# Optimization experiments

Measured on AMD Instinct MI355X. Metric: run time of the kernel, lower is better.

## Reference

```python
import jax, jax.numpy as jnp
import numpy as np

N_X, N_UNITS, N_Y, N_U = 64, 256, 32, 64
BATCH = 32768


def setup_inputs() -> dict:
    key = jax.random.key(0)
    ks = jax.random.split(key, 10)
    nz = 2 * N_X + N_UNITS
    return {
        "u": jax.random.normal(ks[0], (BATCH, N_U, 1), dtype=jnp.float32),
        "x0": jax.random.normal(ks[1], (BATCH, N_X, 1), dtype=jnp.float32),
        # learned parameters (scaled down so H stays well-conditioned and tanh unsaturated)
        "B_2": 0.1 * jax.random.normal(ks[2], (N_X, N_U), dtype=jnp.float32),
        "C_2": 0.1 * jax.random.normal(ks[3], (N_Y, N_X), dtype=jnp.float32),
        "D_12": 0.1 * jax.random.normal(ks[4], (N_UNITS, N_U), dtype=jnp.float32),
        "D_21": 0.1 * jax.random.normal(ks[5], (N_Y, N_UNITS), dtype=jnp.float32),
        "b": 0.1 * jax.random.normal(ks[6], (N_X + N_UNITS + N_Y, 1), dtype=jnp.float32),
        "X": (1.0 / np.sqrt(nz)) * jax.random.normal(ks[7], (nz, nz), dtype=jnp.float32),
        "Y1": 0.1 * jax.random.normal(ks[8], (N_X, N_X), dtype=jnp.float32),
        # fixed IQC multipliers (train_qsr=False): Q nsd, R=I so Rinv=I; S stored transposed
        "S_t": 0.1 * jax.random.normal(ks[9], (N_U, N_Y), dtype=jnp.float32),
        "Q": -jnp.eye(N_Y, dtype=jnp.float32),
        "Rinv": jnp.eye(N_U, dtype=jnp.float32),
    }


def _constrained_weights(B_2, C_2, D_12, D_21, X, S_t, Q, Rinv):
    """Port of REN.updateConstrainedWeights (train_qsr=False). Returns C_1, D_11, lam."""
    n_x, n_units = B_2.shape[0], D_12.shape[0]
    n_y = C_2.shape[0]
    nz = 2 * n_x + n_units
    C2_ = S_t @ C_2                       # [n_u, n_x]
    D21_ = S_t @ D_21 - D_12.T            # [n_u, n_units]
    H = X.T @ X + 1e-3 * jnp.eye(nz, dtype=X.dtype)
    lT1 = jnp.concatenate([C2_.T, D21_.T, B_2], axis=0)          # [nz, n_u]
    H = H + lT1 @ Rinv @ lT1.T
    lT2 = jnp.concatenate([C_2.T, D_21.T, jnp.zeros((n_x, n_y), dtype=X.dtype)], axis=0)
    H = H - lT2 @ Q @ lT2.T
    H_21 = H[n_x:n_x + n_units, :n_x]
    H_22 = H[n_x:n_x + n_units, n_x:n_x + n_units]
    C_1 = -H_21                           # [n_units, n_x]
    lam = 0.5 * jnp.diag(H_22)            # Lambda diagonal, > 0 since H is PD
    # L = tril(-(H_22 - diag(H_22))) == -strictly_lower(H_22)
    D_11 = -jnp.tril(H_22, k=-1)          # strictly lower triangular [n_units, n_units]
    return C_1, D_11, lam


def _forward(u, x0, B_2, C_2, D_12, D_21, b, X, Y1, S_t, Q, Rinv):
    n_x, n_units = B_2.shape[0], D_12.shape[0]
    C_1, D_11, lam = _constrained_weights(B_2, C_2, D_12, D_21, X, S_t, Q, Rinv)
    u2 = u[:, :, 0]                       # [B, n_u]
    x2 = x0[:, :, 0]                      # [B, n_x]
    b_w = b[n_x:n_x + n_units, 0]         # [n_units]
    b_y = b[n_x + n_units:, 0]            # [n_y]
    # precompute the non-recurrent part of the pre-activation for all units
    v = x2 @ C_1.T + u2 @ D_12.T + b_w    # [B, n_units]
    # NOTE: the source uses D_11 row (i_unit - 1), not i_unit (faithful to original code).
    # For i=0 the source uses term2 = 0; D_11 is strictly lower so the full-row dot
    # against the partially-filled w (zeros beyond index i) matches D_11[i-1, :i] @ w[:i].
    Drows = jnp.concatenate([jnp.zeros((1, n_units), dtype=D_11.dtype), D_11[:-1]], axis=0)
    batch = u2.shape[0]

    def step(w, i):
        wi = jnp.tanh((v[:, i] + w @ Drows[i]) / lam[i])   # [B]
        w = w.at[:, i].set(wi)
        return w, None

    w0 = jnp.zeros((batch, n_units), dtype=v.dtype)
    w, _ = jax.lax.scan(step, w0, jnp.arange(n_units))
    y = x2 @ C_2.T + w @ D_21.T + b_y     # [B, n_y]
    return y[:, :, None]                  # [B, n_y, 1]


def reference(u, x0, B_2, C_2, D_12, D_21, b, X, Y1, S_t, Q, Rinv):
    return _forward(u, x0, B_2, C_2, D_12, D_21, b, X, Y1, S_t, Q, Rinv)
```

## Files before the change

kernel.cpp:

```cpp
#include <hip/hip_runtime.h>
#include <hip/hip_bf16.h>

typedef __attribute__((ext_vector_type(8))) short short8;
typedef __attribute__((ext_vector_type(4))) float floatx4;
typedef __attribute__((ext_vector_type(2))) float floatx2;

#define MFMA16 __builtin_amdgcn_mfma_f32_16x16x32_bf16

__device__ inline unsigned short bf16_rn(float f) {
    return (unsigned short)((__float_as_uint(f) + 0x8000u) >> 16);
}
__device__ inline short8 pack8(const float* v) {
    union { short8 s; unsigned int u[4]; } r;
#pragma unroll
    for (int j = 0; j < 4; j++) {
        union { __hip_bfloat162 h; unsigned int u; } c;
        c.h = __float22bfloat162_rn(make_float2(v[2 * j], v[2 * j + 1]));
        r.u[j] = c.u;
    }
    return r.s;
}

__global__ __launch_bounds__(64) void ren_prep13(
    const float* __restrict__ B2, const float* __restrict__ C2,
    const float* __restrict__ D12, const float* __restrict__ D21,
    const float* __restrict__ St, const float* __restrict__ Q,
    const float* __restrict__ Rinv,
    float* __restrict__ lT1, float* __restrict__ t1,
    float* __restrict__ lT2, float* __restrict__ t2,
    unsigned short* __restrict__ Wvb, unsigned short* __restrict__ C2b,
    unsigned short* __restrict__ D21b)
{
    const int t = threadIdx.x;
    const int blk = blockIdx.x;
    if (blk >= 384) {
        const int id = (blk - 384) * 64 + t;
        if (id < 16384) {
            Wvb[(id >> 6) * 128 + 64 + (id & 63)] = bf16_rn(D12[id]);
        } else if (id < 16384 + 2048) {
            C2b[id - 16384] = bf16_rn(C2[id - 16384]);
        } else if (id < 16384 + 2048 + 8192) {
            D21b[id - 18432] = bf16_rn(D21[id - 18432]);
        }
        return;
    }

    __shared__ float stl[64 * 33];
    __shared__ float colbuf[32];
    __shared__ float s1[64];

    const int r = blk;
    const int c = t;
#pragma unroll
    for (int j = 0; j < 32; j++) {
        const int id = j * 64 + t;
        stl[(id >> 5) * 33 + (id & 31)] = St[id];
    }
    if (t < 32)
        colbuf[t] = (r < 64) ? C2[t * 64 + r]
                  : (r < 320 ? D21[t * 256 + (r - 64)] : 0.f);
    __syncthreads();

    float v1;
    if (r < 64) {
        float s = 0.f;
#pragma unroll
        for (int p = 0; p < 32; p++) s += stl[c * 33 + p] * colbuf[p];
        v1 = s;
    } else if (r < 320) {
        float s = 0.f;
#pragma unroll
        for (int p = 0; p < 32; p++) s += stl[c * 33 + p] * colbuf[p];
        v1 = s - D12[(r - 64) * 64 + c];
    } else {
        v1 = B2[(r - 320) * 64 + c];
    }
    s1[c] = v1;
    lT1[r * 64 + c] = v1;
    if (c < 32) {
        const float v2 = (r < 320) ? colbuf[c] : 0.f;
        lT2[r * 32 + c] = v2;
    }
    __syncthreads();

    float a = 0.f;
#pragma unroll
    for (int k = 0; k < 64; k++) a += s1[k] * Rinv[k * 64 + c];
    t1[r * 64 + c] = a;

    if (c < 32) {
        float bq = 0.f;
#pragma unroll
        for (int k = 0; k < 32; k++) bq += colbuf[k] * Q[k * 32 + c];
        t2[r * 32 + c] = bq;
    }
}

__global__ __launch_bounds__(320) void ren_prep2(
    const float* __restrict__ X,
    const float* __restrict__ lT1, const float* __restrict__ t1,
    const float* __restrict__ lT2, const float* __restrict__ t2,
    unsigned short* __restrict__ Wvb, unsigned short* __restrict__ Drowsb,
    float* __restrict__ Dpair, float* __restrict__ lamg)
{
    __shared__ float xcol[384];
    const int c = threadIdx.x;
    const int i = blockIdx.x;
    for (int t = c; t < 384; t += 320) xcol[t] = X[t * 384 + 64 + i];
    __syncthreads();

    float f0 = 0.f, f1 = 0.f, f2 = 0.f, f3 = 0.f;
    float ac[8], au[8], bc8[8], bu[8];
#pragma unroll
    for (int kk = 0; kk < 8; kk++) { ac[kk] = X[kk * 384 + c]; au[kk] = xcol[kk]; }
    for (int k0 = 0; k0 < 384; k0 += 16) {
#pragma unroll
        for (int kk = 0; kk < 8; kk++) {
            bc8[kk] = X[(k0 + 8 + kk) * 384 + c]; bu[kk] = xcol[k0 + 8 + kk];
        }
        f0 += au[0] * ac[0]; f1 += au[1] * ac[1];
        f2 += au[2] * ac[2]; f3 += au[3] * ac[3];
        f0 += au[4] * ac[4]; f1 += au[5] * ac[5];
        f2 += au[6] * ac[6]; f3 += au[7] * ac[7];
        if (k0 + 16 < 384) {
#pragma unroll
            for (int kk = 0; kk < 8; kk++) {
                ac[kk] = X[(k0 + 16 + kk) * 384 + c]; au[kk] = xcol[k0 + 16 + kk];
            }
        }
        f0 += bu[0] * bc8[0]; f1 += bu[1] * bc8[1];
        f2 += bu[2] * bc8[2]; f3 += bu[3] * bc8[3];
        f0 += bu[4] * bc8[4]; f1 += bu[5] * bc8[5];
        f2 += bu[6] * bc8[6]; f3 += bu[7] * bc8[7];
    }

    const float* __restrict__ t1r = t1 + (64 + i) * 64;
    const float* __restrict__ l1r = lT1 + c * 64;
#pragma unroll
    for (int m4 = 0; m4 < 16; m4++) {
        const float4 lv = *(const float4*)(l1r + m4 * 4);
        f0 += t1r[m4 * 4 + 0] * lv.x; f1 += t1r[m4 * 4 + 1] * lv.y;
        f2 += t1r[m4 * 4 + 2] * lv.z; f3 += t1r[m4 * 4 + 3] * lv.w;
    }
    const float* __restrict__ t2r = t2 + (64 + i) * 32;
    const float* __restrict__ l2r = lT2 + c * 32;
#pragma unroll
    for (int m4 = 0; m4 < 8; m4++) {
        const float4 lv = *(const float4*)(l2r + m4 * 4);
        f0 -= t2r[m4 * 4 + 0] * lv.x; f1 -= t2r[m4 * 4 + 1] * lv.y;
        f2 -= t2r[m4 * 4 + 2] * lv.z; f3 -= t2r[m4 * 4 + 3] * lv.w;
    }
    float acc = (f0 + f1) + (f2 + f3) + (((64 + i) == c) ? 0.001f : 0.f);

    if (c < 64) {
        Wvb[i * 128 + c] = bf16_rn(-acc);
    } else {
        const int cb = c - 64;
        if (cb == i) lamg[i] = 5.7707801635558536f / acc;
        if (i < 255) {
            const float dv = (cb <= i - 1) ? -acc : 0.f;
            Drowsb[(i + 1) * 256 + cb] = bf16_rn(dv);
            const int row = i + 1;
            if ((row >> 4) == (cb >> 4)) {
                const int q = row & 15, p = cb & 15;
                Dpair[(row >> 4) * 256 + (q >> 1) * 32 + p * 2 + (q & 1)] = dv;
            }
        } else {
            Drowsb[cb] = 0;
        }
    }
}

__global__ __launch_bounds__(64) void ren_main(
    const float* __restrict__ u, const float* __restrict__ x0,
    const float* __restrict__ b,
    const unsigned short* __restrict__ Wvb,
    const unsigned short* __restrict__ Drowsb,
    const float* __restrict__ Dpair,
    const float* __restrict__ lamg,
    const unsigned short* __restrict__ C2b,
    const unsigned short* __restrict__ D21b,
    float* __restrict__ out)
{
    __shared__ float buf[2][16][20];
    __shared__ float dblk[2][256];
    __shared__ float lamsh[256];
    __shared__ float bsh[256];

    const int L = threadIdx.x;
    const int col = L & 15;
    const int quad = L >> 4;
    const int row0 = blockIdx.x * 16;

#pragma unroll
    for (int j = 0; j < 4; j++) {
        lamsh[j * 64 + L] = lamg[j * 64 + L];
        bsh[j * 64 + L]   = b[64 + j * 64 + L];
    }

    short8 zf[4];
#pragma unroll
    for (int c = 0; c < 4; c++) {
        const float* p = (c < 2 ? x0 : u) + (long)(row0 + col) * 64 + (c & 1) * 32 + quad * 8;
        float t[8];
        *(float4*)&t[0] = *(const float4*)p;
        *(float4*)&t[4] = *(const float4*)(p + 4);
        zf[c] = pack8(t);
    }

    const short8 zero8 = {0, 0, 0, 0, 0, 0, 0, 0};
    short8 wf[8];
#pragma unroll
    for (int c = 0; c < 8; c++) wf[c] = zero8;

    float4 dcur = *(const float4*)(Dpair + 4 * L);
    floatx4 acc0 = {0.f, 0.f, 0.f, 0.f}, acc1 = {0.f, 0.f, 0.f, 0.f};
    {
        short8 v0 = *(const short8*)(Wvb + col * 128 + quad * 8);
        short8 v1 = *(const short8*)(Wvb + col * 128 + 32 + quad * 8);
        short8 v2 = *(const short8*)(Wvb + col * 128 + 64 + quad * 8);
        short8 v3 = *(const short8*)(Wvb + col * 128 + 96 + quad * 8);
        acc0 = MFMA16(zf[0], v0, acc0, 0, 0, 0);
        acc1 = MFMA16(zf[1], v1, acc1, 0, 0, 0);
        acc0 = MFMA16(zf[2], v2, acc0, 0, 0, 0);
        acc1 = MFMA16(zf[3], v3, acc1, 0, 0, 0);
    }

    short8 yc[4];

#pragma unroll
    for (int n = 0; n < 16; n++) {
        const int pp = n & 1;

        short8 vfN[4], hfN[8];
        float4 dnxt;
        if (n < 15) {
            dnxt = *(const float4*)(Dpair + (n + 1) * 256 + 4 * L);
#pragma unroll
            for (int c = 0; c < 4; c++)
                vfN[c] = *(const short8*)(Wvb + (16 * (n + 1) + col) * 128 + c * 32 + quad * 8);
#pragma unroll
            for (int c = 0; c < 8; c++)
                if (c < ((n + 2) >> 1))
                    hfN[c] = *(const short8*)(Drowsb + (16 * (n + 1) + col) * 256 + c * 32 + quad * 8);
        } else {
            yc[0] = *(const short8*)(C2b + col * 64 + quad * 8);
            yc[1] = *(const short8*)(C2b + col * 64 + 32 + quad * 8);
            yc[2] = *(const short8*)(C2b + (16 + col) * 64 + quad * 8);
            yc[3] = *(const short8*)(C2b + (16 + col) * 64 + 32 + quad * 8);
        }

        *(float4*)&dblk[pp][4 * L] = dcur;
        const float bwv = bsh[16 * n + col];
#pragma unroll
        for (int r = 0; r < 4; r++)
            buf[pp][quad * 4 + r][col] = acc0[r] + acc1[r] + bwv;

        float vl[16];
#pragma unroll
        for (int p4 = 0; p4 < 4; p4++)
            *(float4*)&vl[p4 * 4] = *(const float4*)&buf[pp][col][p4 * 4];

        float wl[16];
#pragma unroll
        for (int tq = 0; tq < 8; tq++) {
            floatx2 a2;
            a2[0] = vl[2 * tq]; a2[1] = vl[2 * tq + 1];
#pragma unroll
            for (int p4 = 0; p4 < tq; p4++) {
                const float4 d4 = *(const float4*)&dblk[pp][tq * 32 + p4 * 4];
                floatx2 de; de[0] = d4.x; de[1] = d4.y;
                floatx2 dz; dz[0] = d4.z; dz[1] = d4.w;
                a2 += de * wl[2 * p4];
                a2 += dz * wl[2 * p4 + 1];
            }
            const float2 lmp = *(const float2*)&lamsh[16 * n + 2 * tq];
            floatx2 lm2; lm2[0] = lmp.x; lm2[1] = lmp.y;
            a2 *= lm2;
            const float e0 = __builtin_amdgcn_exp2f(a2[0]);
            const float e1 = __builtin_amdgcn_exp2f(a2[1]);
            wl[2 * tq]     = 1.f - 2.f * __builtin_amdgcn_rcpf(e0 + 1.f);
            wl[2 * tq + 1] = 1.f - 2.f * __builtin_amdgcn_rcpf(e1 + 1.f);
        }

        {
            const short8 nf = pack8(&wl[(quad & 1) * 8]);
            const int cc = n >> 1;
            if ((n & 1) == 0) wf[cc] = (quad < 2) ? nf : zero8;
            else if (quad >= 2) wf[cc] = nf;
        }

        if (n < 15) {
            floatx4 a0 = {0.f, 0.f, 0.f, 0.f}, a1 = {0.f, 0.f, 0.f, 0.f};
            a0 = MFMA16(zf[0], vfN[0], a0, 0, 0, 0);
            a1 = MFMA16(zf[1], vfN[1], a1, 0, 0, 0);
            a0 = MFMA16(zf[2], vfN[2], a0, 0, 0, 0);
            a1 = MFMA16(zf[3], vfN[3], a1, 0, 0, 0);
#pragma unroll
            for (int c = 0; c < 8; c++)
                if (c < ((n + 2) >> 1)) {
                    if (c & 1) a1 = MFMA16(wf[c], hfN[c], a1, 0, 0, 0);
                    else       a0 = MFMA16(wf[c], hfN[c], a0, 0, 0, 0);
                }
            acc0 = a0; acc1 = a1;
            dcur = dnxt;
        }
    }

    floatx4 y0 = {0.f, 0.f, 0.f, 0.f}, y1 = {0.f, 0.f, 0.f, 0.f};
    y0 = MFMA16(zf[0], yc[0], y0, 0, 0, 0);
    y1 = MFMA16(zf[0], yc[2], y1, 0, 0, 0);
    y0 = MFMA16(zf[1], yc[1], y0, 0, 0, 0);
    y1 = MFMA16(zf[1], yc[3], y1, 0, 0, 0);
#pragma unroll
    for (int c = 0; c < 8; c++) {
        const short8 b0 = *(const short8*)(D21b + col * 256 + c * 32 + quad * 8);
        const short8 b1 = *(const short8*)(D21b + (16 + col) * 256 + c * 32 + quad * 8);
        y0 = MFMA16(wf[c], b0, y0, 0, 0, 0);
        y1 = MFMA16(wf[c], b1, y1, 0, 0, 0);
    }
    const float by0 = b[320 + col];
    const float by1 = b[336 + col];
#pragma unroll
    for (int r = 0; r < 4; r++) {
        out[(long)(row0 + quad * 4 + r) * 32 + col]      = y0[r] + by0;
        out[(long)(row0 + quad * 4 + r) * 32 + 16 + col] = y1[r] + by1;
    }
}

extern "C" void kernel_launch(void* const* d_in, const int* in_sizes, int n_in,
                              void* d_out, int out_size, void* d_ws, size_t ws_size,
                              hipStream_t stream)
{
    const float* u    = (const float*)d_in[0];
    const float* x0   = (const float*)d_in[1];
    const float* B2   = (const float*)d_in[2];
    const float* C2   = (const float*)d_in[3];
    const float* D12  = (const float*)d_in[4];
    const float* D21  = (const float*)d_in[5];
    const float* b    = (const float*)d_in[6];
    const float* X    = (const float*)d_in[7];
    const float* St   = (const float*)d_in[9];
    const float* Q    = (const float*)d_in[10];
    const float* Rinv = (const float*)d_in[11];
    float* out = (float*)d_out;

    float* ws     = (float*)d_ws;
    float* lT1    = ws;
    float* t1     = lT1 + 384 * 64;
    float* lT2    = t1 + 384 * 64;
    float* t2     = lT2 + 384 * 32;
    float* lamg   = t2 + 384 * 32;
    float* Dpair  = lamg + 256;
    unsigned short* Drowsb = (unsigned short*)(Dpair + 16 * 256);
    unsigned short* Wvb    = Drowsb + 256 * 256;
    unsigned short* C2b    = Wvb + 256 * 128;
    unsigned short* D21b   = C2b + 32 * 64;

    ren_prep13<<<dim3(800), dim3(64), 0, stream>>>(B2, C2, D12, D21, St, Q, Rinv,
                                                   lT1, t1, lT2, t2, Wvb, C2b, D21b);
    ren_prep2<<<dim3(256), dim3(320), 0, stream>>>(X, lT1, t1, lT2, t2,
                                                   Wvb, Drowsb, Dpair, lamg);

    const int batch = in_sizes[0] / 64;
    ren_main<<<dim3(batch / 16), dim3(64), 0, stream>>>(u, x0, b, Wvb, Drowsb,
                                                        Dpair, lamg, C2b, D21b, out);
}
```

Baseline: 141.3 us.

## Share staged weight blocks across four waves via LDS double buffering

The main kernel grows from one wave per block to four waves (256 threads). The per-step weight fragments (Wv, Drows band, Dpair) are repacked in the prep kernels into one contiguous pre-swizzled staging layout. Each block cooperatively loads the next step's slab into a double-buffered shared-memory array, and every wave reads its MFMA operands from LDS. This cuts redundant global and L2 weight traffic per batch row, at the cost of a block-wide barrier every step and more LDS per block, which may limit occupancy.

```diff
diff --git a/kernel.cpp b/kernel.cpp
--- a/kernel.cpp
+++ b/kernel.cpp
@@ -6,6 +6,8 @@
 typedef __attribute__((ext_vector_type(2))) float floatx2;
 
 #define MFMA16 __builtin_amdgcn_mfma_f32_16x16x32_bf16
+
+#define BASEF4(n) (320 * (n) + 64 * ((((n) * (n))) >> 2))
 
 __device__ inline unsigned short bf16_rn(float f) {
     return (unsigned short)((__float_as_uint(f) + 0x8000u) >> 16);
@@ -28,7 +30,7 @@
     const float* __restrict__ Rinv,
     float* __restrict__ lT1, float* __restrict__ t1,
     float* __restrict__ lT2, float* __restrict__ t2,
-    unsigned short* __restrict__ Wvb, unsigned short* __restrict__ C2b,
+    unsigned short* __restrict__ stgS, unsigned short* __restrict__ C2b,
     unsigned short* __restrict__ D21b)
 {
     const int t = threadIdx.x;
@@ -36,7 +38,11 @@
     if (blk >= 384) {
         const int id = (blk - 384) * 64 + t;
         if (id < 16384) {
-            Wvb[(id >> 6) * 128 + 64 + (id & 63)] = bf16_rn(D12[id]);
+            const int i = id >> 6, k = id & 63;
+            const int n = i >> 4, r = i & 15;
+            const int cc = 2 + (k >> 5), kk = k & 31;
+            stgS[(BASEF4(n) + cc * 64 + (kk >> 3) * 16 + r) * 8 + (kk & 7)] =
+                bf16_rn(D12[id]);
         } else if (id < 16384 + 2048) {
             C2b[id - 16384] = bf16_rn(C2[id - 16384]);
         } else if (id < 16384 + 2048 + 8192) {
@@ -100,8 +106,7 @@
     const float* __restrict__ X,
     const float* __restrict__ lT1, const float* __restrict__ t1,
     const float* __restrict__ lT2, const float* __restrict__ t2,
-    unsigned short* __restrict__ Wvb, unsigned short* __restrict__ Drowsb,
-    float* __restrict__ Dpair, float* __restrict__ lamg)
+    float* __restrict__ stgF, float* __restrict__ lamg)
 {
     __shared__ float xcol[384];
     const int c = threadIdx.x;
@@ -152,97 +157,88 @@
     }
     float acc = (f0 + f1) + (f2 + f3) + (((64 + i) == c) ? 0.001f : 0.f);
 
+    unsigned short* stgS = (unsigned short*)stgF;
     if (c < 64) {
-        Wvb[i * 128 + c] = bf16_rn(-acc);
+        const int n = i >> 4, r = i & 15;
+        const int cc = c >> 5, kk = c & 31;
+        stgS[(BASEF4(n) + cc * 64 + (kk >> 3) * 16 + r) * 8 + (kk & 7)] =
+            bf16_rn(-acc);
     } else {
         const int cb = c - 64;
         if (cb == i) lamg[i] = 5.7707801635558536f / acc;
         if (i < 255) {
+            const int row = i + 1, n = row >> 4, r = row & 15;
+            const int cN = (n + 1) >> 1;
             const float dv = (cb <= i - 1) ? -acc : 0.f;
-            Drowsb[(i + 1) * 256 + cb] = bf16_rn(dv);
-            const int row = i + 1;
-            if ((row >> 4) == (cb >> 4)) {
-                const int q = row & 15, p = cb & 15;
-                Dpair[(row >> 4) * 256 + (q >> 1) * 32 + p * 2 + (q & 1)] = dv;
-            }
-        } else {
-            Drowsb[cb] = 0;
-        }
-    }
-}
-
-__global__ __launch_bounds__(64) void ren_main(
+            if (cb < cN * 32) {
+                const int cc = cb >> 5, kk = cb & 31;
+                stgS[(BASEF4(n) + 256 + cc * 64 + (kk >> 3) * 16 + r) * 8 + (kk & 7)] =
+                    bf16_rn(dv);
+            }
+            if ((cb >> 4) == (row >> 4)) {
+                stgF[(BASEF4(n) + 256 + cN * 64) * 4 +
+                     (r >> 1) * 32 + (cb & 15) * 2 + (r & 1)] = dv;
+            }
+        }
+    }
+}
+
+__global__ __launch_bounds__(256, 2) void ren_main(
     const float* __restrict__ u, const float* __restrict__ x0,
     const float* __restrict__ b,
-    const unsigned short* __restrict__ Wvb,
-    const unsigned short* __restrict__ Drowsb,
-    const float* __restrict__ Dpair,
+    const float4* __restrict__ stg,
     const float* __restrict__ lamg,
     const unsigned short* __restrict__ C2b,
     const unsigned short* __restrict__ D21b,
     float* __restrict__ out)
 {
-    __shared__ float buf[2][16][20];
-    __shared__ float dblk[2][256];
+    __shared__ float4 sbuf[2][832];
+    __shared__ float tbuf[4][16][20];
     __shared__ float lamsh[256];
     __shared__ float bsh[256];
 
-    const int L = threadIdx.x;
-    const int col = L & 15;
-    const int quad = L >> 4;
-    const int row0 = blockIdx.x * 16;
-
-#pragma unroll
-    for (int j = 0; j < 4; j++) {
-        lamsh[j * 64 + L] = lamg[j * 64 + L];
-        bsh[j * 64 + L]   = b[64 + j * 64 + L];
-    }
+    const int tid = threadIdx.x;
+    const int L = tid & 63, wid = tid >> 6;
+    const int col = L & 15, quad = L >> 4;
+    const long row0 = (long)blockIdx.x * 64 + wid * 16;
+
+    lamsh[tid] = lamg[tid];
+    bsh[tid]   = b[64 + tid];
 
     short8 zf[4];
 #pragma unroll
     for (int c = 0; c < 4; c++) {
-        const float* p = (c < 2 ? x0 : u) + (long)(row0 + col) * 64 + (c & 1) * 32 + quad * 8;
+        const float* p = (c < 2 ? x0 : u) + (row0 + col) * 64 + (c & 1) * 32 + quad * 8;
         float t[8];
         *(float4*)&t[0] = *(const float4*)p;
         *(float4*)&t[4] = *(const float4*)(p + 4);
         zf[c] = pack8(t);
     }
 
+    sbuf[0][tid] = stg[tid];
+    if (tid < 64) sbuf[0][256 + tid] = stg[256 + tid];
+    __syncthreads();
+
     const short8 zero8 = {0, 0, 0, 0, 0, 0, 0, 0};
     short8 wf[8];
 #pragma unroll
     for (int c = 0; c < 8; c++) wf[c] = zero8;
 
-    float4 dcur = *(const float4*)(Dpair + 4 * L);
-    floatx4 acc0 = {0.f, 0.f, 0.f, 0.f}, acc1 = {0.f, 0.f, 0.f, 0.f};
-    {
-        short8 v0 = *(const short8*)(Wvb + col * 128 + quad * 8);
-        short8 v1 = *(const short8*)(Wvb + col * 128 + 32 + quad * 8);
-        short8 v2 = *(const short8*)(Wvb + col * 128 + 64 + quad * 8);
-        short8 v3 = *(const short8*)(Wvb + col * 128 + 96 + quad * 8);
-        acc0 = MFMA16(zf[0], v0, acc0, 0, 0, 0);
-        acc1 = MFMA16(zf[1], v1, acc1, 0, 0, 0);
-        acc0 = MFMA16(zf[2], v2, acc0, 0, 0, 0);
-        acc1 = MFMA16(zf[3], v3, acc1, 0, 0, 0);
-    }
-
     short8 yc[4];
 
 #pragma unroll
     for (int n = 0; n < 16; n++) {
-        const int pp = n & 1;
-
-        short8 vfN[4], hfN[8];
-        float4 dnxt;
+        const int cur = n & 1, nxt = cur ^ 1;
+        const int cN = (n + 1) >> 1;
+        if (n > 0) __syncthreads();
+
+        float4 st[4];
+        const int totN = 320 + ((n + 2) >> 1) * 64;
         if (n < 15) {
-            dnxt = *(const float4*)(Dpair + (n + 1) * 256 + 4 * L);
-#pragma unroll
-            for (int c = 0; c < 4; c++)
-                vfN[c] = *(const short8*)(Wvb + (16 * (n + 1) + col) * 128 + c * 32 + quad * 8);
-#pragma unroll
-            for (int c = 0; c < 8; c++)
-                if (c < ((n + 2) >> 1))
-                    hfN[c] = *(const short8*)(Drowsb + (16 * (n + 1) + col) * 256 + c * 32 + quad * 8);
+#pragma unroll
+            for (int r = 0; r < 4; r++)
+                if (r * 256 + tid < totN)
+                    st[r] = stg[BASEF4(n + 1) + r * 256 + tid];
         } else {
             yc[0] = *(const short8*)(C2b + col * 64 + quad * 8);
             yc[1] = *(const short8*)(C2b + col * 64 + 32 + quad * 8);
@@ -250,17 +246,37 @@
             yc[3] = *(const short8*)(C2b + (16 + col) * 64 + 32 + quad * 8);
         }
 
-        *(float4*)&dblk[pp][4 * L] = dcur;
+        const float4* sb = sbuf[cur];
+        floatx4 acc0 = {0.f, 0.f, 0.f, 0.f}, acc1 = {0.f, 0.f, 0.f, 0.f};
+        {
+            const short8 v0 = *(const short8*)&sb[0 * 64 + L];
+            const short8 v1 = *(const short8*)&sb[1 * 64 + L];
+            const short8 v2 = *(const short8*)&sb[2 * 64 + L];
+            const short8 v3 = *(const short8*)&sb[3 * 64 + L];
+            acc0 = MFMA16(zf[0], v0, acc0, 0, 0, 0);
+            acc1 = MFMA16(zf[1], v1, acc1, 0, 0, 0);
+            acc0 = MFMA16(zf[2], v2, acc0, 0, 0, 0);
+            acc1 = MFMA16(zf[3], v3, acc1, 0, 0, 0);
+        }
+#pragma unroll
+        for (int c = 0; c < 8; c++)
+            if (c < cN) {
+                const short8 hb = *(const short8*)&sb[256 + c * 64 + L];
+                if (c & 1) acc1 = MFMA16(wf[c], hb, acc1, 0, 0, 0);
+                else       acc0 = MFMA16(wf[c], hb, acc0, 0, 0, 0);
+            }
+
         const float bwv = bsh[16 * n + col];
 #pragma unroll
         for (int r = 0; r < 4; r++)
-            buf[pp][quad * 4 + r][col] = acc0[r] + acc1[r] + bwv;
+            tbuf[wid][quad * 4 + r][col] = acc0[r] + acc1[r] + bwv;
 
         float vl[16];
 #pragma unroll
         for (int p4 = 0; p4 < 4; p4++)
-            *(float4*)&vl[p4 * 4] = *(const float4*)&buf[pp][col][p4 * 4];
-
+            *(float4*)&vl[p4 * 4] = *(const float4*)&tbuf[wid][col][p4 * 4];
+
+        const float* dpr = (const float*)(sb + 256 + cN * 64);
         float wl[16];
 #pragma unroll
         for (int tq = 0; tq < 8; tq++) {
@@ -268,7 +284,7 @@
             a2[0] = vl[2 * tq]; a2[1] = vl[2 * tq + 1];
 #pragma unroll
             for (int p4 = 0; p4 < tq; p4++) {
-                const float4 d4 = *(const float4*)&dblk[pp][tq * 32 + p4 * 4];
+                const float4 d4 = *(const float4*)&dpr[tq * 32 + p4 * 4];
                 floatx2 de; de[0] = d4.x; de[1] = d4.y;
                 floatx2 dz; dz[0] = d4.z; dz[1] = d4.w;
                 a2 += de * wl[2 * p4];
@@ -291,19 +307,10 @@
         }
 
         if (n < 15) {
-            floatx4 a0 = {0.f, 0.f, 0.f, 0.f}, a1 = {0.f, 0.f, 0.f, 0.f};
-            a0 = MFMA16(zf[0], vfN[0], a0, 0, 0, 0);
-            a1 = MFMA16(zf[1], vfN[1], a1, 0, 0, 0);
-            a0 = MFMA16(zf[2], vfN[2], a0, 0, 0, 0);
-            a1 = MFMA16(zf[3], vfN[3], a1, 0, 0, 0);
-#pragma unroll
-            for (int c = 0; c < 8; c++)
-                if (c < ((n + 2) >> 1)) {
-                    if (c & 1) a1 = MFMA16(wf[c], hfN[c], a1, 0, 0, 0);
-                    else       a0 = MFMA16(wf[c], hfN[c], a0, 0, 0, 0);
-                }
-            acc0 = a0; acc1 = a1;
-            dcur = dnxt;
+#pragma unroll
+            for (int r = 0; r < 4; r++)
+                if (r * 256 + tid < totN)
+                    sbuf[nxt][r * 256 + tid] = st[r];
         }
     }
 
@@ -323,8 +330,8 @@
     const float by1 = b[336 + col];
 #pragma unroll
     for (int r = 0; r < 4; r++) {
-        out[(long)(row0 + quad * 4 + r) * 32 + col]      = y0[r] + by0;
-        out[(long)(row0 + quad * 4 + r) * 32 + 16 + col] = y1[r] + by1;
+        out[(row0 + quad * 4 + r) * 32 + col]      = y0[r] + by0;
+        out[(row0 + quad * 4 + r) * 32 + 16 + col] = y1[r] + by1;
     }
 }
 
@@ -345,24 +352,23 @@
     const float* Rinv = (const float*)d_in[11];
     float* out = (float*)d_out;
 
-    float* ws     = (float*)d_ws;
-    float* lT1    = ws;
+    float4* stg   = (float4*)d_ws;
+    float*  fbase = (float*)(stg + 9216);
+    float* lT1    = fbase;
     float* t1     = lT1 + 384 * 64;
     float* lT2    = t1 + 384 * 64;
     float* t2     = lT2 + 384 * 32;
     float* lamg   = t2 + 384 * 32;
-    float* Dpair  = lamg + 256;
-    unsigned short* Drowsb = (unsigned short*)(Dpair + 16 * 256);
-    unsigned short* Wvb    = Drowsb + 256 * 256;
-    unsigned short* C2b    = Wvb + 256 * 128;
-    unsigned short* D21b   = C2b + 32 * 64;
+    unsigned short* C2b  = (unsigned short*)(lamg + 256);
+    unsigned short* D21b = C2b + 32 * 64;
 
     ren_prep13<<<dim3(800), dim3(64), 0, stream>>>(B2, C2, D12, D21, St, Q, Rinv,
-                                                   lT1, t1, lT2, t2, Wvb, C2b, D21b);
+                                                   lT1, t1, lT2, t2,
+                                                   (unsigned short*)stg, C2b, D21b);
     ren_prep2<<<dim3(256), dim3(320), 0, stream>>>(X, lT1, t1, lT2, t2,
-                                                   Wvb, Drowsb, Dpair, lamg);
+                                                   (float*)stg, lamg);
 
     const int batch = in_sizes[0] / 64;
-    ren_main<<<dim3(batch / 16), dim3(64), 0, stream>>>(u, x0, b, Wvb, Drowsb,
-                                                        Dpair, lamg, C2b, D21b, out);
-}
+    ren_main<<<dim3(batch / 64), dim3(256), 0, stream>>>(u, x0, b, stg, lamg,
+                                                         C2b, D21b, out);
+}
```

Result: slower. 151.8 us (+7.4%).

## Use 32-wide diagonal blocks and precompute all input projections up front

Applied to the files above, without the earlier changes.

The triangular recurrence now works on 8 diagonal blocks of 32 units instead of 16 blocks of 16. All input-projection MFMAs run up front into 16 accumulators. After each block is solved, its contribution is pushed forward into every later block's accumulator with MFMAs, instead of recomputing the full prefix each step. This roughly halves the number of serial block steps and removes redundant MFMA work, at the cost of a longer scalar triangular solve per block (32 sequential tanh per lane-row) and more accumulator registers.

```diff
diff --git a/kernel.cpp b/kernel.cpp
--- a/kernel.cpp
+++ b/kernel.cpp
@@ -101,7 +101,7 @@
     const float* __restrict__ lT1, const float* __restrict__ t1,
     const float* __restrict__ lT2, const float* __restrict__ t2,
     unsigned short* __restrict__ Wvb, unsigned short* __restrict__ Drowsb,
-    float* __restrict__ Dpair, float* __restrict__ lamg)
+    float* __restrict__ Dsup, float* __restrict__ lamg)
 {
     __shared__ float xcol[384];
     const int c = threadIdx.x;
@@ -157,13 +157,14 @@
     } else {
         const int cb = c - 64;
         if (cb == i) lamg[i] = 5.7707801635558536f / acc;
+        if (i == 0 && cb < 32) Dsup[cb * 2] = 0.f;
         if (i < 255) {
             const float dv = (cb <= i - 1) ? -acc : 0.f;
             Drowsb[(i + 1) * 256 + cb] = bf16_rn(dv);
             const int row = i + 1;
-            if ((row >> 4) == (cb >> 4)) {
-                const int q = row & 15, p = cb & 15;
-                Dpair[(row >> 4) * 256 + (q >> 1) * 32 + p * 2 + (q & 1)] = dv;
+            if ((cb >> 5) == (row >> 5)) {
+                const int q = row & 31, p = cb & 31;
+                Dsup[(row >> 5) * 1024 + (q >> 1) * 64 + p * 2 + (q & 1)] = dv;
             }
         } else {
             Drowsb[cb] = 0;
@@ -176,21 +177,21 @@
     const float* __restrict__ b,
     const unsigned short* __restrict__ Wvb,
     const unsigned short* __restrict__ Drowsb,
-    const float* __restrict__ Dpair,
+    const float* __restrict__ Dsup,
     const float* __restrict__ lamg,
     const unsigned short* __restrict__ C2b,
     const unsigned short* __restrict__ D21b,
     float* __restrict__ out)
 {
-    __shared__ float buf[2][16][20];
-    __shared__ float dblk[2][256];
+    __shared__ float dblk[1024];
+    __shared__ float tbuf[16][40];
     __shared__ float lamsh[256];
     __shared__ float bsh[256];
 
     const int L = threadIdx.x;
     const int col = L & 15;
     const int quad = L >> 4;
-    const int row0 = blockIdx.x * 16;
+    const long row0 = (long)blockIdx.x * 16;
 
 #pragma unroll
     for (int j = 0; j < 4; j++) {
@@ -201,80 +202,69 @@
     short8 zf[4];
 #pragma unroll
     for (int c = 0; c < 4; c++) {
-        const float* p = (c < 2 ? x0 : u) + (long)(row0 + col) * 64 + (c & 1) * 32 + quad * 8;
+        const float* p = (c < 2 ? x0 : u) + (row0 + col) * 64 + (c & 1) * 32 + quad * 8;
         float t[8];
         *(float4*)&t[0] = *(const float4*)p;
         *(float4*)&t[4] = *(const float4*)(p + 4);
         zf[c] = pack8(t);
     }
 
-    const short8 zero8 = {0, 0, 0, 0, 0, 0, 0, 0};
+    floatx4 accA[8], accB[8];
+#pragma unroll
+    for (int N = 0; N < 8; N++) {
+        floatx4 a = {0.f, 0.f, 0.f, 0.f}, bb = {0.f, 0.f, 0.f, 0.f};
+#pragma unroll
+        for (int c = 0; c < 4; c++) {
+            const short8 fA = *(const short8*)(Wvb + (32 * N + col) * 128 + c * 32 + quad * 8);
+            const short8 fB = *(const short8*)(Wvb + (32 * N + 16 + col) * 128 + c * 32 + quad * 8);
+            a  = MFMA16(zf[c], fA, a, 0, 0, 0);
+            bb = MFMA16(zf[c], fB, bb, 0, 0, 0);
+        }
+        accA[N] = a; accB[N] = bb;
+    }
+
     short8 wf[8];
-#pragma unroll
-    for (int c = 0; c < 8; c++) wf[c] = zero8;
-
-    float4 dcur = *(const float4*)(Dpair + 4 * L);
-    floatx4 acc0 = {0.f, 0.f, 0.f, 0.f}, acc1 = {0.f, 0.f, 0.f, 0.f};
-    {
-        short8 v0 = *(const short8*)(Wvb + col * 128 + quad * 8);
-        short8 v1 = *(const short8*)(Wvb + col * 128 + 32 + quad * 8);
-        short8 v2 = *(const short8*)(Wvb + col * 128 + 64 + quad * 8);
-        short8 v3 = *(const short8*)(Wvb + col * 128 + 96 + quad * 8);
-        acc0 = MFMA16(zf[0], v0, acc0, 0, 0, 0);
-        acc1 = MFMA16(zf[1], v1, acc1, 0, 0, 0);
-        acc0 = MFMA16(zf[2], v2, acc0, 0, 0, 0);
-        acc1 = MFMA16(zf[3], v3, acc1, 0, 0, 0);
-    }
-
-    short8 yc[4];
-
-#pragma unroll
-    for (int n = 0; n < 16; n++) {
-        const int pp = n & 1;
-
-        short8 vfN[4], hfN[8];
-        float4 dnxt;
-        if (n < 15) {
-            dnxt = *(const float4*)(Dpair + (n + 1) * 256 + 4 * L);
-#pragma unroll
-            for (int c = 0; c < 4; c++)
-                vfN[c] = *(const short8*)(Wvb + (16 * (n + 1) + col) * 128 + c * 32 + quad * 8);
-#pragma unroll
-            for (int c = 0; c < 8; c++)
-                if (c < ((n + 2) >> 1))
-                    hfN[c] = *(const short8*)(Drowsb + (16 * (n + 1) + col) * 256 + c * 32 + quad * 8);
-        } else {
-            yc[0] = *(const short8*)(C2b + col * 64 + quad * 8);
-            yc[1] = *(const short8*)(C2b + col * 64 + 32 + quad * 8);
-            yc[2] = *(const short8*)(C2b + (16 + col) * 64 + quad * 8);
-            yc[3] = *(const short8*)(C2b + (16 + col) * 64 + 32 + quad * 8);
-        }
-
-        *(float4*)&dblk[pp][4 * L] = dcur;
-        const float bwv = bsh[16 * n + col];
-#pragma unroll
-        for (int r = 0; r < 4; r++)
-            buf[pp][quad * 4 + r][col] = acc0[r] + acc1[r] + bwv;
-
-        float vl[16];
-#pragma unroll
-        for (int p4 = 0; p4 < 4; p4++)
-            *(float4*)&vl[p4 * 4] = *(const float4*)&buf[pp][col][p4 * 4];
-
-        float wl[16];
-#pragma unroll
-        for (int tq = 0; tq < 8; tq++) {
+    const float4* Dsup4 = (const float4*)Dsup;
+
+#pragma unroll
+    for (int N = 0; N < 8; N++) {
+        float4 dv0 = Dsup4[N * 256 + 0 * 64 + L];
+        float4 dv1 = Dsup4[N * 256 + 1 * 64 + L];
+        float4 dv2 = Dsup4[N * 256 + 2 * 64 + L];
+        float4 dv3 = Dsup4[N * 256 + 3 * 64 + L];
+        ((float4*)dblk)[0 * 64 + L] = dv0;
+        ((float4*)dblk)[1 * 64 + L] = dv1;
+        ((float4*)dblk)[2 * 64 + L] = dv2;
+        ((float4*)dblk)[3 * 64 + L] = dv3;
+
+        const float bwA = bsh[32 * N + col];
+        const float bwB = bsh[32 * N + 16 + col];
+#pragma unroll
+        for (int r = 0; r < 4; r++) {
+            tbuf[quad * 4 + r][col]      = accA[N][r] + bwA;
+            tbuf[quad * 4 + r][20 + col] = accB[N][r] + bwB;
+        }
+        float vl[32];
+#pragma unroll
+        for (int p4 = 0; p4 < 4; p4++) {
+            *(float4*)&vl[p4 * 4]      = *(const float4*)&tbuf[col][p4 * 4];
+            *(float4*)&vl[16 + p4 * 4] = *(const float4*)&tbuf[col][20 + p4 * 4];
+        }
+
+        float wl[32];
+#pragma unroll
+        for (int tq = 0; tq < 16; tq++) {
             floatx2 a2;
             a2[0] = vl[2 * tq]; a2[1] = vl[2 * tq + 1];
 #pragma unroll
             for (int p4 = 0; p4 < tq; p4++) {
-                const float4 d4 = *(const float4*)&dblk[pp][tq * 32 + p4 * 4];
+                const float4 d4 = *(const float4*)&dblk[tq * 64 + p4 * 4];
                 floatx2 de; de[0] = d4.x; de[1] = d4.y;
                 floatx2 dz; dz[0] = d4.z; dz[1] = d4.w;
                 a2 += de * wl[2 * p4];
                 a2 += dz * wl[2 * p4 + 1];
             }
-            const float2 lmp = *(const float2*)&lamsh[16 * n + 2 * tq];
+            const float2 lmp = *(const float2*)&lamsh[32 * N + 2 * tq];
             floatx2 lm2; lm2[0] = lmp.x; lm2[1] = lmp.y;
             a2 *= lm2;
             const float e0 = __builtin_amdgcn_exp2f(a2[0]);
@@ -283,35 +273,25 @@
             wl[2 * tq + 1] = 1.f - 2.f * __builtin_amdgcn_rcpf(e1 + 1.f);
         }
 
-        {
-            const short8 nf = pack8(&wl[(quad & 1) * 8]);
-            const int cc = n >> 1;
-            if ((n & 1) == 0) wf[cc] = (quad < 2) ? nf : zero8;
-            else if (quad >= 2) wf[cc] = nf;
-        }
-
-        if (n < 15) {
-            floatx4 a0 = {0.f, 0.f, 0.f, 0.f}, a1 = {0.f, 0.f, 0.f, 0.f};
-            a0 = MFMA16(zf[0], vfN[0], a0, 0, 0, 0);
-            a1 = MFMA16(zf[1], vfN[1], a1, 0, 0, 0);
-            a0 = MFMA16(zf[2], vfN[2], a0, 0, 0, 0);
-            a1 = MFMA16(zf[3], vfN[3], a1, 0, 0, 0);
-#pragma unroll
-            for (int c = 0; c < 8; c++)
-                if (c < ((n + 2) >> 1)) {
-                    if (c & 1) a1 = MFMA16(wf[c], hfN[c], a1, 0, 0, 0);
-                    else       a0 = MFMA16(wf[c], hfN[c], a0, 0, 0, 0);
-                }
-            acc0 = a0; acc1 = a1;
-            dcur = dnxt;
+        wf[N] = pack8(&wl[quad * 8]);
+
+#pragma unroll
+        for (int M = N + 1; M < 8; M++) {
+            const short8 hA = *(const short8*)(Drowsb + (32 * M + col) * 256 + N * 32 + quad * 8);
+            const short8 hB = *(const short8*)(Drowsb + (32 * M + 16 + col) * 256 + N * 32 + quad * 8);
+            accA[M] = MFMA16(wf[N], hA, accA[M], 0, 0, 0);
+            accB[M] = MFMA16(wf[N], hB, accB[M], 0, 0, 0);
         }
     }
 
     floatx4 y0 = {0.f, 0.f, 0.f, 0.f}, y1 = {0.f, 0.f, 0.f, 0.f};
-    y0 = MFMA16(zf[0], yc[0], y0, 0, 0, 0);
-    y1 = MFMA16(zf[0], yc[2], y1, 0, 0, 0);
-    y0 = MFMA16(zf[1], yc[1], y0, 0, 0, 0);
-    y1 = MFMA16(zf[1], yc[3], y1, 0, 0, 0);
+#pragma unroll
+    for (int c = 0; c < 2; c++) {
+        const short8 b0 = *(const short8*)(C2b + col * 64 + c * 32 + quad * 8);
+        const short8 b1 = *(const short8*)(C2b + (16 + col) * 64 + c * 32 + quad * 8);
+        y0 = MFMA16(zf[c], b0, y0, 0, 0, 0);
+        y1 = MFMA16(zf[c], b1, y1, 0, 0, 0);
+    }
 #pragma unroll
     for (int c = 0; c < 8; c++) {
         const short8 b0 = *(const short8*)(D21b + col * 256 + c * 32 + quad * 8);
@@ -323,8 +303,8 @@
     const float by1 = b[336 + col];
 #pragma unroll
     for (int r = 0; r < 4; r++) {
-        out[(long)(row0 + quad * 4 + r) * 32 + col]      = y0[r] + by0;
-        out[(long)(row0 + quad * 4 + r) * 32 + 16 + col] = y1[r] + by1;
+        out[(row0 + quad * 4 + r) * 32 + col]      = y0[r] + by0;
+        out[(row0 + quad * 4 + r) * 32 + 16 + col] = y1[r] + by1;
     }
 }
 
@@ -351,8 +331,8 @@
     float* lT2    = t1 + 384 * 64;
     float* t2     = lT2 + 384 * 32;
     float* lamg   = t2 + 384 * 32;
-    float* Dpair  = lamg + 256;
-    unsigned short* Drowsb = (unsigned short*)(Dpair + 16 * 256);
+    float* Dsup   = lamg + 256;
+    unsigned short* Drowsb = (unsigned short*)(Dsup + 8 * 1024);
     unsigned short* Wvb    = Drowsb + 256 * 256;
     unsigned short* C2b    = Wvb + 256 * 128;
     unsigned short* D21b   = C2b + 32 * 64;
@@ -360,9 +340,9 @@
     ren_prep13<<<dim3(800), dim3(64), 0, stream>>>(B2, C2, D12, D21, St, Q, Rinv,
                                                    lT1, t1, lT2, t2, Wvb, C2b, D21b);
     ren_prep2<<<dim3(256), dim3(320), 0, stream>>>(X, lT1, t1, lT2, t2,
-                                                   Wvb, Drowsb, Dpair, lamg);
+                                                   Wvb, Drowsb, Dsup, lamg);
 
     const int batch = in_sizes[0] / 64;
     ren_main<<<dim3(batch / 16), dim3(64), 0, stream>>>(u, x0, b, Wvb, Drowsb,
-                                                        Dpair, lamg, C2b, D21b, out);
-}
+                                                        Dsup, lamg, C2b, D21b, out);
+}
```

New measurement: 271.5 us. 1.92x slower.
